# Kernel optimization log

Measured on AMD Instinct MI355X. Metric: run time of the kernel, lower is better.

Reference implementation:

```python
import jax, jax.numpy as jnp
import numpy as np

B, NNEG, D, E = 16384, 10, 8, 64
N_ENT = 500000  # sum(domain_dims.values())
N_PAIRS = D * (D - 1) // 2


def setup_inputs() -> dict:
    key = jax.random.key(0)
    k1, k2, k3, k4, k5 = jax.random.split(key, 5)
    return {
        "pos_x": jax.random.randint(k1, (B, D), 0, N_ENT, dtype=jnp.int32),
        "neg_x": jax.random.randint(k2, (B, NNEG, D), 0, N_ENT, dtype=jnp.int32),
        "emb_table": jax.random.normal(k3, (N_ENT, E), dtype=jnp.float32) * 0.01,
        "pair_w": jax.random.uniform(k4, (N_PAIRS,), dtype=jnp.float32),
        "c": jax.random.uniform(k5, (1,), dtype=jnp.float32),
    }


def _obtain_score(x, emb_table, pair_w, c):
    # x: [..., D] int indices into the shared embedding table
    e = emb_table[x]                                   # [..., D, E] gather
    gram = jnp.einsum('...de,...fe->...df', e, e)      # [..., D, D] pairwise dots
    iu, ju = np.triu_indices(D, k=1)
    pair_dots = gram[..., iu, ju]                      # [..., N_PAIRS]
    # NOTE: the original torch code never increments k inside obtain_score,
    # so EVERY pair is scaled by exp(pair_W['0']). We replicate that faithfully.
    r = pair_dots * jnp.exp(pair_w[0])
    return jnp.exp(jnp.sum(r, axis=-1) + c[0])         # [...]


def reference(pos_x, neg_x, emb_table, pair_w, c):
    pos_score = _obtain_score(pos_x, emb_table, pair_w, c)   # [B]
    # vectorized over the negative-sample axis (original loops in Python)
    neg_score = _obtain_score(neg_x, emb_table, pair_w, c)   # [B, NNEG]
    return pos_score, neg_score
```

## Files before the change

### kernel.cpp

```cpp
#include <hip/hip_runtime.h>

constexpr int B     = 16384;
constexpr int NNEG  = 10;
constexpr int D     = 8;
constexpr int E     = 64;
constexpr int ROWS  = B * (1 + NNEG);

__global__ __launch_bounds__(256) void APE_61555471286335_kernel(
    const int*   __restrict__ pos_x,
    const int*   __restrict__ neg_x,
    const float* __restrict__ emb,
    const float* __restrict__ pair_w,
    const float* __restrict__ c,
    float*       __restrict__ out)
{
    const int wave = (int)((blockIdx.x * blockDim.x + threadIdx.x) >> 6);
    const int lane = threadIdx.x & 63;
    if (wave >= ROWS) return;

    const int* idx = (wave < B) ? (pos_x + (size_t)wave * D)
                                : (neg_x + (size_t)(wave - B) * D);

    float s = 0.0f, ss = 0.0f;
#pragma unroll
    for (int d = 0; d < D; ++d) {
        const int id = idx[d];
        const float v = emb[(size_t)id * E + lane];
        s  += v;
        ss += v * v;
    }

    float a = s * s;
#pragma unroll
    for (int off = 32; off > 0; off >>= 1) {
        a  += __shfl_xor(a,  off, 64);
        ss += __shfl_xor(ss, off, 64);
    }

    if (lane == 0) {
        const float pair_sum = 0.5f * (a - ss);
        out[wave] = expf(pair_sum * expf(pair_w[0]) + c[0]);
    }
}

extern "C" void kernel_launch(void* const* d_in, const int* in_sizes, int n_in,
                              void* d_out, int out_size, void* d_ws, size_t ws_size,
                              hipStream_t stream) {
    const int*   pos_x  = (const int*)  d_in[0];
    const int*   neg_x  = (const int*)  d_in[1];
    const float* emb    = (const float*)d_in[2];
    const float* pair_w = (const float*)d_in[3];
    const float* c      = (const float*)d_in[4];
    float*       out    = (float*)      d_out;

    constexpr int BLOCK = 256;
    constexpr int WAVES_PER_BLOCK = BLOCK / 64;
    const int grid = (ROWS + WAVES_PER_BLOCK - 1) / WAVES_PER_BLOCK;

    APE_61555471286335_kernel<<<grid, BLOCK, 0, stream>>>(
        pos_x, neg_x, emb, pair_w, c, out);
}
```

Measured before the change: 220.3 us.

## Process eight rows per wave with vectorized float4 embedding loads

Each wave now handles eight rows instead of one. Each 8-lane group reads one row's indices with two int4 loads and fetches 8 floats per lane per embedding row as two float4 loads. This cuts per-row index-load latency, replaces the 64-lane reductions with 3-step shuffles, and gives each lane more independent loads in flight. The random gather is still memory-bound, so the gain depends on better latency hiding. Each 8-lane group now reads a 256-byte row, where before a whole wave read it coalesced.

```diff
diff --git a/kernel.cpp b/kernel.cpp
--- a/kernel.cpp
+++ b/kernel.cpp
@@ -5,6 +5,7 @@
 constexpr int D     = 8;
 constexpr int E     = 64;
 constexpr int ROWS  = B * (1 + NNEG);
+constexpr int RPW   = 8;
 
 __global__ __launch_bounds__(256) void APE_61555471286335_kernel(
     const int*   __restrict__ pos_x,
@@ -14,32 +15,47 @@
     const float* __restrict__ c,
     float*       __restrict__ out)
 {
-    const int wave = (int)((blockIdx.x * blockDim.x + threadIdx.x) >> 6);
+    const int tid  = blockIdx.x * blockDim.x + threadIdx.x;
+    const int wave = tid >> 6;
     const int lane = threadIdx.x & 63;
-    if (wave >= ROWS) return;
+    const int g    = lane >> 3;
+    const int t    = lane & 7;
+    const int row  = wave * RPW + g;
 
-    const int* idx = (wave < B) ? (pos_x + (size_t)wave * D)
-                                : (neg_x + (size_t)(wave - B) * D);
+    const int* idx = (row < B) ? (pos_x + (size_t)row * D)
+                               : (neg_x + (size_t)(row - B) * D);
+    const int4 i0 = *(const int4*)(idx);
+    const int4 i1 = *(const int4*)(idx + 4);
+    const int ids[D] = {i0.x, i0.y, i0.z, i0.w, i1.x, i1.y, i1.z, i1.w};
 
-    float s = 0.0f, ss = 0.0f;
+    float4 s0 = make_float4(0.f, 0.f, 0.f, 0.f), s1 = s0;
+    float4 q0 = s0, q1 = s0;
 #pragma unroll
     for (int d = 0; d < D; ++d) {
-        const int id = idx[d];
-        const float v = emb[(size_t)id * E + lane];
-        s  += v;
-        ss += v * v;
+        const float* r = emb + (size_t)ids[d] * E + t * 8;
+        const float4 v0 = *(const float4*)(r);
+        const float4 v1 = *(const float4*)(r + 4);
+        s0.x += v0.x; s0.y += v0.y; s0.z += v0.z; s0.w += v0.w;
+        s1.x += v1.x; s1.y += v1.y; s1.z += v1.z; s1.w += v1.w;
+        q0.x += v0.x * v0.x; q0.y += v0.y * v0.y;
+        q0.z += v0.z * v0.z; q0.w += v0.w * v0.w;
+        q1.x += v1.x * v1.x; q1.y += v1.y * v1.y;
+        q1.z += v1.z * v1.z; q1.w += v1.w * v1.w;
     }
 
-    float a = s * s;
+    float a = s0.x * s0.x + s0.y * s0.y + s0.z * s0.z + s0.w * s0.w
+            + s1.x * s1.x + s1.y * s1.y + s1.z * s1.z + s1.w * s1.w;
+    float q = q0.x + q0.y + q0.z + q0.w + q1.x + q1.y + q1.z + q1.w;
+
 #pragma unroll
-    for (int off = 32; off > 0; off >>= 1) {
-        a  += __shfl_xor(a,  off, 64);
-        ss += __shfl_xor(ss, off, 64);
+    for (int off = 4; off > 0; off >>= 1) {
+        a += __shfl_xor(a, off, 64);
+        q += __shfl_xor(q, off, 64);
     }
 
-    if (lane == 0) {
-        const float pair_sum = 0.5f * (a - ss);
-        out[wave] = expf(pair_sum * expf(pair_w[0]) + c[0]);
+    if (t == 0) {
+        const float pair_sum = 0.5f * (a - q);
+        out[row] = expf(pair_sum * expf(pair_w[0]) + c[0]);
     }
 }
 
@@ -54,8 +70,9 @@
     float*       out    = (float*)      d_out;
 
     constexpr int BLOCK = 256;
-    constexpr int WAVES_PER_BLOCK = BLOCK / 64;
-    const int grid = (ROWS + WAVES_PER_BLOCK - 1) / WAVES_PER_BLOCK;
+    constexpr int ROWS_PER_BLOCK = (BLOCK / 64) * RPW;
+    static_assert(ROWS % ROWS_PER_BLOCK == 0, "exact grid");
+    const int grid = ROWS / ROWS_PER_BLOCK;
 
     APE_61555471286335_kernel<<<grid, BLOCK, 0, stream>>>(
         pos_x, neg_x, emb, pair_w, c, out);
```

Result: slower. 240.3 us (+9.1%).
